# Performance work log

Measured on AMD Instinct MI355X. Metric: run time of the kernel, lower is better.

Reference implementation:

```python
import jax, jax.numpy as jnp
import numpy as np

N_NODES = 100000
N_EDGES = 1600000
UNITS = 256
N_LAYERS = 4          # model_layers
NUM_GRAPHS = 512
IN_FEAT = 9


def _glorot(key, shape):
    lim = float(np.sqrt(6.0 / (shape[0] + shape[1])))
    return jax.random.uniform(key, shape, jnp.float32, -lim, lim)


def setup_inputs() -> dict:
    key = jax.random.key(0)
    ks = jax.random.split(key, 16)
    x = jax.random.normal(ks[0], (N_NODES, IN_FEAT), jnp.float32)
    edge_index = jax.random.randint(ks[1], (2, N_EDGES), 0, N_NODES, jnp.int64)
    batch = jnp.sort(jax.random.randint(ks[2], (N_NODES,), 0, NUM_GRAPHS, jnp.int64))
    Win = _glorot(ks[3], (IN_FEAT, UNITS))
    bin_ = jnp.zeros((UNITS,), jnp.float32)
    Ws = jnp.stack([_glorot(ks[4 + i], (UNITS, UNITS)) for i in range(N_LAYERS - 1)])
    bs = jnp.zeros((N_LAYERS - 1, UNITS), jnp.float32)
    fc1_w = _glorot(ks[8], (UNITS, UNITS))
    fc1_b = jnp.zeros((UNITS,), jnp.float32)
    fc2_w = _glorot(ks[9], (UNITS, 32))
    fc2_b = jnp.zeros((32,), jnp.float32)
    fc3_w = _glorot(ks[10], (32, 1))
    fc3_b = jnp.zeros((1,), jnp.float32)
    return dict(x=x, edge_index=edge_index, batch=batch, Win=Win, bin_=bin_,
                Ws=Ws, bs=bs, fc1_w=fc1_w, fc1_b=fc1_b, fc2_w=fc2_w,
                fc2_b=fc2_b, fc3_w=fc3_w, fc3_b=fc3_b)


def _gcn_conv(x, W, b, src, dst, dinv):
    # PyG GCNConv: h = xW ; out = D^-1/2 (A+I) D^-1/2 h + b  (self-loops added)
    h = x @ W                                     # [N, d]
    norm = dinv[src] * dinv[dst]                  # [E]
    agg = jnp.zeros_like(h).at[dst].add(h[src] * norm[:, None])
    agg = agg + h * (dinv * dinv)[:, None]        # self-loop term
    return agg + b


def reference(x, edge_index, batch, Win, bin_, Ws, bs,
              fc1_w, fc1_b, fc2_w, fc2_b, fc3_w, fc3_b):
    src, dst = edge_index[0], edge_index[1]
    # degree with self-loops
    deg = jnp.zeros((N_NODES,), jnp.float32).at[dst].add(1.0) + 1.0
    dinv = jax.lax.rsqrt(deg)

    h = jnp.tanh(_gcn_conv(x, Win, bin_, src, dst, dinv))
    for i in range(N_LAYERS - 1):
        h = jnp.tanh(_gcn_conv(h, Ws[i], bs[i], src, dst, dinv))
        # dropout: identity at inference
    h = jnp.tanh(h @ fc1_w + fc1_b)
    h = jnp.tanh(h @ fc2_w + fc2_b)
    h = h @ fc3_w + fc3_b                          # [N, 1]
    # global mean pool over graphs
    sums = jax.ops.segment_sum(h, batch, num_segments=NUM_GRAPHS)      # [G, 1]
    cnts = jax.ops.segment_sum(jnp.ones((N_NODES,), jnp.float32), batch,
                               num_segments=NUM_GRAPHS)
    pooled = sums / jnp.maximum(cnts, 1.0)[:, None]
    return jax.nn.sigmoid(pooled)
```

## Files before the change

### kernel.cpp

```cpp
#include <hip/hip_runtime.h>
#include <math.h>

#define N_NODES 100000
#define N_EDGES 1600000
#define UNITS   256
#define NGRAPH  512
#define IN_FEAT 9
#define NB_SCAN ((N_NODES + 255) / 256)
#define NBUK    ((N_NODES + 255) / 256)
#define BCAP    8192
#define EPB     4096
#define NPB     ((N_EDGES + EPB - 1) / EPB)

typedef short bf16x8 __attribute__((ext_vector_type(8)));
typedef float f32x4  __attribute__((ext_vector_type(4)));
typedef float f32x2  __attribute__((ext_vector_type(2)));

__device__ __forceinline__ float bflo(unsigned int u) {
  return __builtin_bit_cast(float, u << 16);
}
__device__ __forceinline__ float bfhi(unsigned int u) {
  return __builtin_bit_cast(float, u & 0xffff0000u);
}
__device__ __forceinline__ unsigned short f2bf(float f) {
  unsigned int u = __builtin_bit_cast(unsigned int, f);
  u += 0x7fffu + ((u >> 16) & 1u);
  return (unsigned short)(u >> 16);
}

__device__ __forceinline__ bf16x8 f8tobf(uint2 q) {
  f32x2 v0 = __builtin_amdgcn_cvt_pk_f32_fp8(q.x, false);
  f32x2 v1 = __builtin_amdgcn_cvt_pk_f32_fp8(q.x, true);
  f32x2 v2 = __builtin_amdgcn_cvt_pk_f32_fp8(q.y, false);
  f32x2 v3 = __builtin_amdgcn_cvt_pk_f32_fp8(q.y, true);
  bf16x8 a;
  a[0] = (short)f2bf(v0[0]); a[1] = (short)f2bf(v0[1]);
  a[2] = (short)f2bf(v1[0]); a[3] = (short)f2bf(v1[1]);
  a[4] = (short)f2bf(v2[0]); a[5] = (short)f2bf(v2[1]);
  a[6] = (short)f2bf(v3[0]); a[7] = (short)f2bf(v3[1]);
  return a;
}

__device__ __forceinline__ int swz(int row, int byteInRow) {
  return row * 128 + (byteInRow ^ ((row & 7) << 4));
}
__device__ __forceinline__ int swzA(int row, int byteInRow) {
  return row * 512 + (byteInRow ^ ((row & 7) << 4));
}


__global__ __launch_bounds__(256) void k_part(const int* __restrict__ ei,
                                              int* __restrict__ bcnt,
                                              uint2* __restrict__ bstore) {
  __shared__ int hist[NBUK];
  __shared__ int base[NBUK];
  int tid = threadIdx.x;
  int e0 = blockIdx.x * EPB;
  for (int i = tid; i < NBUK; i += 256) hist[i] = 0;
  __syncthreads();
  #pragma unroll 4
  for (int j = 0; j < EPB / 256; ++j) {
    int e = e0 + j * 256 + tid;
    if (e < N_EDGES) atomicAdd(&hist[ei[N_EDGES + e] >> 8], 1);
  }
  __syncthreads();
  for (int i = tid; i < NBUK; i += 256) {
    int h = hist[i];
    base[i] = h ? atomicAdd(&bcnt[i], h) : 0;
    hist[i] = 0;
  }
  __syncthreads();
  #pragma unroll 4
  for (int j = 0; j < EPB / 256; ++j) {
    int e = e0 + j * 256 + tid;
    if (e < N_EDGES) {
      int s = ei[e];
      int d = ei[N_EDGES + e];
      int b = d >> 8;
      int pos = base[b] + atomicAdd(&hist[b], 1);
      bstore[(size_t)b * BCAP + pos] = make_uint2((unsigned)s, (unsigned)d);
    }
  }
}

__global__ __launch_bounds__(256) void k_cnt(const int* __restrict__ bcnt,
                                             const uint2* __restrict__ bstore,
                                             int* __restrict__ cnt) {
  __shared__ int h[256];
  int b = blockIdx.x, tid = threadIdx.x;
  h[tid] = 0;
  __syncthreads();
  int nE = bcnt[b];
  for (int i = tid; i < nE; i += 256)
    atomicAdd(&h[bstore[(size_t)b * BCAP + i].y & 255], 1);
  __syncthreads();
  int node = b * 256 + tid;
  if (node < N_NODES) cnt[node] = h[tid];
}

__global__ __launch_bounds__(256) void k_colfill(const int* __restrict__ bcnt,
                                                 const uint2* __restrict__ bstore,
                                                 const int* __restrict__ row_ptr,
                                                 int* __restrict__ col) {
  __shared__ int cur[256];
  int b = blockIdx.x, tid = threadIdx.x;
  int node = b * 256 + tid;
  cur[tid] = (node < N_NODES) ? row_ptr[node] : 0;
  __syncthreads();
  int nE = bcnt[b];
  for (int i = tid; i < nE; i += 256) {
    uint2 sd = bstore[(size_t)b * BCAP + i];
    int pos = atomicAdd(&cur[sd.y & 255], 1);
    col[pos] = (int)sd.x;
  }
}

__global__ __launch_bounds__(256) void k_bsum(const int* __restrict__ cnt,
                                              int* __restrict__ bsum) {
  __shared__ int wsS[4];
  int b = blockIdx.x, tid = threadIdx.x, lane = tid & 63, w = tid >> 6;
  int idx = b * 256 + tid;
  int s = (idx < N_NODES) ? cnt[idx] : 0;
  #pragma unroll
  for (int m = 32; m >= 1; m >>= 1) s += __shfl_xor(s, m);
  if (lane == 0) wsS[w] = s;
  __syncthreads();
  if (tid == 0) bsum[b] = wsS[0] + wsS[1] + wsS[2] + wsS[3];
}

__global__ __launch_bounds__(512) void k_bscan(int* __restrict__ bsum) {
  __shared__ int wsS[8];
  int tid = threadIdx.x, lane = tid & 63, w = tid >> 6;
  int v = (tid < NB_SCAN) ? bsum[tid] : 0;
  int s = v;
  #pragma unroll
  for (int off = 1; off < 64; off <<= 1) {
    int t = __shfl_up(s, off);
    if (lane >= off) s += t;
  }
  if (lane == 63) wsS[w] = s;
  __syncthreads();
  int woff = 0;
  #pragma unroll
  for (int i = 0; i < 8; ++i) woff += (i < w) ? wsS[i] : 0;
  if (tid < NB_SCAN) bsum[tid] = woff + s - v;
}

__global__ __launch_bounds__(256) void k_scan3(const int* __restrict__ cnt,
                                               const int* __restrict__ bsum,
                                               int* __restrict__ row_ptr,
                                               float* __restrict__ dinv) {
  __shared__ int wsS[4];
  int b = blockIdx.x, tid = threadIdx.x, lane = tid & 63, w = tid >> 6;
  int idx = b * 256 + tid;
  int v = (idx < N_NODES) ? cnt[idx] : 0;
  int s = v;
  #pragma unroll
  for (int off = 1; off < 64; off <<= 1) {
    int t = __shfl_up(s, off);
    if (lane >= off) s += t;
  }
  if (lane == 63) wsS[w] = s;
  __syncthreads();
  int woff = 0;
  #pragma unroll
  for (int i = 0; i < 4; ++i) woff += (i < w) ? wsS[i] : 0;
  if (idx < N_NODES) {
    row_ptr[idx] = bsum[b] + woff + s - v;
    dinv[idx] = rsqrtf((float)v + 1.0f);
  }
  if (idx == 0) row_ptr[N_NODES] = N_EDGES;
}

__global__ void k_bounds(const int* __restrict__ batch, int* __restrict__ starts) {
  int g = blockIdx.x * blockDim.x + threadIdx.x;
  if (g > NGRAPH) return;
  if (g == NGRAPH) { starts[g] = N_NODES; return; }
  int lo = 0, hi = N_NODES;
  while (lo < hi) { int m = (lo + hi) >> 1; if (batch[m] < g) lo = m + 1; else hi = m; }
  starts[g] = lo;
}


__global__ void k_cvtW(const float* __restrict__ Ws, const float* __restrict__ fc1_w,
                       unsigned short* __restrict__ Wt) {
  int idx = blockIdx.x * 256 + threadIdx.x;
  int m = idx >> 16;
  int r = idx & 65535;
  int n = r >> 8;
  int k = r & 255;
  const float* src = (m < 3) ? (Ws + (size_t)m * 65536) : fc1_w;
  Wt[idx] = f2bf(src[k * 256 + n]);
}

__global__ void k_cvtW2(const float* __restrict__ fc2_w, unsigned short* __restrict__ Wt2) {
  int idx = blockIdx.x * 256 + threadIdx.x;
  int n = idx >> 8;
  int k = idx & 255;
  Wt2[idx] = f2bf(fc2_w[k * 32 + n]);
}

__global__ void k_scalex(const float* __restrict__ x, const float* __restrict__ dinv,
                         float* __restrict__ xs) {
  int idx = blockIdx.x * blockDim.x + threadIdx.x;
  if (idx < N_NODES * IN_FEAT) xs[idx] = x[idx] * dinv[idx / IN_FEAT];
}


__global__ void k_agg9(const float* __restrict__ xs, const int* __restrict__ row_ptr,
                       const int* __restrict__ col, const float* __restrict__ dinv,
                       float* __restrict__ p0) {
  int n = blockIdx.x * blockDim.x + threadIdx.x;
  if (n >= N_NODES) return;
  float acc[IN_FEAT];
  #pragma unroll
  for (int j = 0; j < IN_FEAT; ++j) acc[j] = xs[n * IN_FEAT + j];
  int beg = row_ptr[n], end = row_ptr[n + 1];
  for (int e = beg; e < end; ++e) {
    int s = col[e];
    #pragma unroll
    for (int j = 0; j < IN_FEAT; ++j) acc[j] += xs[s * IN_FEAT + j];
  }
  float dn = dinv[n];
  #pragma unroll
  for (int j = 0; j < IN_FEAT; ++j) p0[n * IN_FEAT + j] = dn * acc[j];
}

__global__ __launch_bounds__(256) void k_gemm9(const float* __restrict__ p0,
                                               const float* __restrict__ Win,
                                               const float* __restrict__ bin,
                                               const float* __restrict__ scale,
                                               unsigned char* __restrict__ h8) {
  __shared__ float pS[32][IN_FEAT];
  int tid = threadIdx.x;
  int row0 = blockIdx.x * 32;
  for (int i = tid; i < 32 * IN_FEAT; i += 256) {
    int r = i / IN_FEAT;
    pS[r][i % IN_FEAT] = (row0 + r < N_NODES) ? p0[(size_t)row0 * IN_FEAT + i] : 0.0f;
  }
  float wcol[IN_FEAT];
  #pragma unroll
  for (int k = 0; k < IN_FEAT; ++k) wcol[k] = Win[k * UNITS + tid];
  float b = bin[tid];
  __syncthreads();
  for (int r = 0; r < 32; ++r) {
    int gr = row0 + r;
    if (gr >= N_NODES) break;
    float a = b;
    #pragma unroll
    for (int k = 0; k < IN_FEAT; ++k) a += pS[r][k] * wcol[k];
    float v = scale[gr] * tanhf(a);
    float vn = __shfl_xor(v, 1);
    if ((tid & 1) == 0) {
      unsigned int pk = __builtin_amdgcn_cvt_pk_fp8_f32(v, vn, 0, false);
      *(unsigned short*)(h8 + (size_t)gr * UNITS + tid) = (unsigned short)pk;
    }
  }
}


__global__ __launch_bounds__(256) void k_agg256(
    const unsigned int* __restrict__ hs8,
    const int* __restrict__ row_ptr, const int* __restrict__ col,
    const float* __restrict__ dinv, unsigned int* __restrict__ p8) {
  int wid = threadIdx.x >> 6;
  int lane = threadIdx.x & 63;
  int n = blockIdx.x * 4 + wid;
  if (n >= N_NODES) return;
  unsigned int q = hs8[(size_t)n * 64 + lane];
  f32x2 lo = __builtin_amdgcn_cvt_pk_f32_fp8(q, false);
  f32x2 hi = __builtin_amdgcn_cvt_pk_f32_fp8(q, true);
  float a0 = lo[0], a1 = lo[1], a2 = hi[0], a3 = hi[1];
  int e = row_ptr[n], end = row_ptr[n + 1];
  for (; e + 8 <= end; e += 8) {
    int s[8];
    unsigned int qq[8];
    #pragma unroll
    for (int j = 0; j < 8; ++j) s[j] = col[e + j];
    #pragma unroll
    for (int j = 0; j < 8; ++j) qq[j] = hs8[(size_t)s[j] * 64 + lane];
    #pragma unroll
    for (int j = 0; j < 8; ++j) {
      f32x2 l2 = __builtin_amdgcn_cvt_pk_f32_fp8(qq[j], false);
      f32x2 h2 = __builtin_amdgcn_cvt_pk_f32_fp8(qq[j], true);
      a0 += l2[0]; a1 += l2[1]; a2 += h2[0]; a3 += h2[1];
    }
  }
  if (e + 4 <= end) {
    int s[4];
    unsigned int qq[4];
    #pragma unroll
    for (int j = 0; j < 4; ++j) s[j] = col[e + j];
    #pragma unroll
    for (int j = 0; j < 4; ++j) qq[j] = hs8[(size_t)s[j] * 64 + lane];
    #pragma unroll
    for (int j = 0; j < 4; ++j) {
      f32x2 l2 = __builtin_amdgcn_cvt_pk_f32_fp8(qq[j], false);
      f32x2 h2 = __builtin_amdgcn_cvt_pk_f32_fp8(qq[j], true);
      a0 += l2[0]; a1 += l2[1]; a2 += h2[0]; a3 += h2[1];
    }
    e += 4;
  }
  for (; e < end; ++e) {
    unsigned int q0 = hs8[(size_t)col[e] * 64 + lane];
    f32x2 l2 = __builtin_amdgcn_cvt_pk_f32_fp8(q0, false);
    f32x2 h2 = __builtin_amdgcn_cvt_pk_f32_fp8(q0, true);
    a0 += l2[0]; a1 += l2[1]; a2 += h2[0]; a3 += h2[1];
  }
  float dn = dinv[n];
  unsigned int u = __builtin_amdgcn_cvt_pk_fp8_f32(dn * a0, dn * a1, 0, false);
  u = __builtin_amdgcn_cvt_pk_fp8_f32(dn * a2, dn * a3, u, true);
  p8[(size_t)n * 64 + lane] = u;
}


__global__ __launch_bounds__(256, 4) void k_gemm_f8(
    const unsigned char* __restrict__ A8,
    const unsigned short* __restrict__ Wt,
    const float* __restrict__ bias,
    const float* __restrict__ scale,
    unsigned char* __restrict__ C8,
    int M) {
  __shared__ __align__(16) char lds[33792];
  char* Bs = lds;
  unsigned short (*Cs)[264] = (unsigned short(*)[264])lds;

  const int tid = threadIdx.x;
  const int w = tid >> 6;
  const int l = tid & 63;
  const int l15 = l & 15;
  const int blk = l >> 4;
  const int wr = w >> 1, wc = w & 1;
  const int row0 = blockIdx.x * 64;

  const int sr = tid >> 3;
  const int sc = (tid & 7) * 16;

  const unsigned char* aRow[2];
  #pragma unroll
  for (int rf = 0; rf < 2; ++rf) {
    int gr = row0 + 32 * wr + rf * 16 + l15;
    if (gr >= M) gr = M - 1;
    aRow[rf] = A8 + (size_t)gr * UNITS + 8 * blk;
  }

  f32x4 acc[2][8];
  #pragma unroll
  for (int rf = 0; rf < 2; ++rf)
    #pragma unroll
    for (int cf = 0; cf < 8; ++cf) acc[rf][cf] = (f32x4){0.f, 0.f, 0.f, 0.f};

  for (int ks = 0; ks < 4; ++ks) {
    const int k0 = ks * 64;
    if (ks) __syncthreads();
    #pragma unroll
    for (int i = 0; i < 8; ++i) {
      int n = sr + i * 32;
      uint4 v = *(const uint4*)(Wt + (size_t)n * UNITS + k0 + (sc >> 1));
      *(uint4*)(Bs + swz(n, sc)) = v;
    }
    __syncthreads();
    #pragma unroll
    for (int kc = 0; kc < 2; ++kc) {
      bf16x8 a[2];
      #pragma unroll
      for (int rf = 0; rf < 2; ++rf) {
        uint2 q = *(const uint2*)(aRow[rf] + k0 + kc * 32);
        a[rf] = f8tobf(q);
      }
      #pragma unroll
      for (int cf = 0; cf < 8; ++cf) {
        bf16x8 b = *(const bf16x8*)(Bs + swz(128 * wc + cf * 16 + l15, kc * 64 + blk * 16));
        acc[0][cf] = __builtin_amdgcn_mfma_f32_16x16x32_bf16(a[0], b, acc[0][cf], 0, 0, 0);
        acc[1][cf] = __builtin_amdgcn_mfma_f32_16x16x32_bf16(a[1], b, acc[1][cf], 0, 0, 0);
      }
    }
  }

  __syncthreads();
  float dvv[2][4];
  #pragma unroll
  for (int rf = 0; rf < 2; ++rf)
    #pragma unroll
    for (int reg = 0; reg < 4; ++reg) {
      int gr = row0 + 32 * wr + rf * 16 + 4 * blk + reg;
      dvv[rf][reg] = scale[gr < M ? gr : M - 1];
    }
  #pragma unroll
  for (int cf = 0; cf < 8; ++cf) {
    float bcol = bias[128 * wc + cf * 16 + l15];
    #pragma unroll
    for (int rf = 0; rf < 2; ++rf) {
      #pragma unroll
      for (int reg = 0; reg < 4; ++reg) {
        float v = dvv[rf][reg] * tanhf(acc[rf][cf][reg] + bcol);
        Cs[32 * wr + rf * 16 + 4 * blk + reg][128 * wc + cf * 16 + l15] = f2bf(v);
      }
    }
  }
  __syncthreads();
  #pragma unroll
  for (int j = 0; j < 8; ++j) {
    int flat = tid + j * 256;
    int r = flat >> 5;
    int c = flat & 31;
    int gr = row0 + r;
    if (gr < M) {
      uint4 v = *(const uint4*)&Cs[r][c * 8];
      uint2 u;
      u.x = __builtin_amdgcn_cvt_pk_fp8_f32(bflo(v.x), bfhi(v.x), 0, false);
      u.x = __builtin_amdgcn_cvt_pk_fp8_f32(bflo(v.y), bfhi(v.y), u.x, true);
      u.y = __builtin_amdgcn_cvt_pk_fp8_f32(bflo(v.z), bfhi(v.z), 0, false);
      u.y = __builtin_amdgcn_cvt_pk_fp8_f32(bflo(v.w), bfhi(v.w), u.y, true);
      *(uint2*)(C8 + (size_t)gr * UNITS + c * 8) = u;
    }
  }
}


__global__ __launch_bounds__(256, 2) void k_mlp(
    const unsigned char* __restrict__ A8,
    const unsigned short* __restrict__ WtL2, const float* __restrict__ bL2,
    const unsigned short* __restrict__ Wtfc1, const float* __restrict__ bfc1,
    const unsigned short* __restrict__ Wt2, const float* __restrict__ b2,
    const float* __restrict__ w3, const float* __restrict__ b3,
    float* __restrict__ ns, int M) {
  __shared__ __align__(16) char lds[65536];
  char* T  = lds;
  char* Bs = lds + 32768;

  const int tid = threadIdx.x;
  const int w = tid >> 6;
  const int l = tid & 63;
  const int l15 = l & 15;
  const int blk = l >> 4;
  const int wr = w >> 1, wc = w & 1;
  const int row0 = blockIdx.x * 64;

  const int sr = tid >> 3;
  const int sc = (tid & 7) * 16;

  const unsigned char* aRow[2];
  #pragma unroll
  for (int rf = 0; rf < 2; ++rf) {
    int gr = row0 + 32 * wr + rf * 16 + l15;
    if (gr >= M) gr = M - 1;
    aRow[rf] = A8 + (size_t)gr * UNITS + 8 * blk;
  }
  f32x4 acc[2][8];
  #pragma unroll
  for (int rf = 0; rf < 2; ++rf)
    #pragma unroll
    for (int cf = 0; cf < 8; ++cf) acc[rf][cf] = (f32x4){0.f, 0.f, 0.f, 0.f};

  for (int ks = 0; ks < 4; ++ks) {
    const int k0 = ks * 64;
    if (ks) __syncthreads();
    #pragma unroll
    for (int i = 0; i < 8; ++i) {
      int n = sr + i * 32;
      uint4 v = *(const uint4*)(WtL2 + (size_t)n * UNITS + k0 + (sc >> 1));
      *(uint4*)(Bs + swz(n, sc)) = v;
    }
    __syncthreads();
    #pragma unroll
    for (int kc = 0; kc < 2; ++kc) {
      bf16x8 a[2];
      #pragma unroll
      for (int rf = 0; rf < 2; ++rf)
        a[rf] = f8tobf(*(const uint2*)(aRow[rf] + k0 + kc * 32));
      #pragma unroll
      for (int cf = 0; cf < 8; ++cf) {
        bf16x8 b = *(const bf16x8*)(Bs + swz(128 * wc + cf * 16 + l15, kc * 64 + blk * 16));
        acc[0][cf] = __builtin_amdgcn_mfma_f32_16x16x32_bf16(a[0], b, acc[0][cf], 0, 0, 0);
        acc[1][cf] = __builtin_amdgcn_mfma_f32_16x16x32_bf16(a[1], b, acc[1][cf], 0, 0, 0);
      }
    }
  }
  #pragma unroll
  for (int cf = 0; cf < 8; ++cf) {
    float bcol = bL2[128 * wc + cf * 16 + l15];
    #pragma unroll
    for (int rf = 0; rf < 2; ++rf) {
      #pragma unroll
      for (int reg = 0; reg < 4; ++reg) {
        int row = 32 * wr + rf * 16 + 4 * blk + reg;
        int colb = (128 * wc + cf * 16 + l15) * 2;
        *(unsigned short*)(T + swzA(row, colb)) = f2bf(tanhf(acc[rf][cf][reg] + bcol));
      }
    }
  }

  #pragma unroll
  for (int rf = 0; rf < 2; ++rf)
    #pragma unroll
    for (int cf = 0; cf < 8; ++cf) acc[rf][cf] = (f32x4){0.f, 0.f, 0.f, 0.f};
  for (int ks = 0; ks < 4; ++ks) {
    const int k0 = ks * 64;
    __syncthreads();
    #pragma unroll
    for (int i = 0; i < 8; ++i) {
      int n = sr + i * 32;
      uint4 v = *(const uint4*)(Wtfc1 + (size_t)n * UNITS + k0 + (sc >> 1));
      *(uint4*)(Bs + swz(n, sc)) = v;
    }
    __syncthreads();
    #pragma unroll
    for (int kc = 0; kc < 2; ++kc) {
      bf16x8 a[2];
      #pragma unroll
      for (int rf = 0; rf < 2; ++rf) {
        int ar = 32 * wr + rf * 16 + l15;
        a[rf] = *(const bf16x8*)(T + swzA(ar, blk * 16 + ks * 128 + kc * 64));
      }
      #pragma unroll
      for (int cf = 0; cf < 8; ++cf) {
        bf16x8 b = *(const bf16x8*)(Bs + swz(128 * wc + cf * 16 + l15, kc * 64 + blk * 16));
        acc[0][cf] = __builtin_amdgcn_mfma_f32_16x16x32_bf16(a[0], b, acc[0][cf], 0, 0, 0);
        acc[1][cf] = __builtin_amdgcn_mfma_f32_16x16x32_bf16(a[1], b, acc[1][cf], 0, 0, 0);
      }
    }
  }

  __syncthreads();
  #pragma unroll
  for (int cf = 0; cf < 8; ++cf) {
    float bcol = bfc1[128 * wc + cf * 16 + l15];
    #pragma unroll
    for (int rf = 0; rf < 2; ++rf) {
      #pragma unroll
      for (int reg = 0; reg < 4; ++reg) {
        int row = 32 * wr + rf * 16 + 4 * blk + reg;
        int colb = (128 * wc + cf * 16 + l15) * 2;
        *(unsigned short*)(T + swzA(row, colb)) = f2bf(tanhf(acc[rf][cf][reg] + bcol));
      }
    }
  }
  #pragma unroll
  for (int i = 0; i < 4; ++i) {
    int idx = tid + i * 256;
    int row = idx >> 5;
    int c = idx & 31;
    uint4 v = *(const uint4*)(Wt2 + (size_t)row * UNITS + c * 8);
    *(uint4*)(Bs + row * 512 + ((c * 16) ^ ((row & 7) << 4))) = v;
  }
  __syncthreads();

  f32x4 acc0 = (f32x4){0.f, 0.f, 0.f, 0.f};
  f32x4 acc1 = (f32x4){0.f, 0.f, 0.f, 0.f};
  #pragma unroll
  for (int k0 = 0; k0 < UNITS; k0 += 32) {
    int byte = k0 * 2 + blk * 16;
    bf16x8 a  = *(const bf16x8*)(T + swzA(16 * w + l15, byte));
    bf16x8 b0 = *(const bf16x8*)(Bs + l15 * 512 + (byte ^ ((l15 & 7) << 4)));
    bf16x8 b1 = *(const bf16x8*)(Bs + (16 + l15) * 512 + (byte ^ ((l15 & 7) << 4)));
    acc0 = __builtin_amdgcn_mfma_f32_16x16x32_bf16(a, b0, acc0, 0, 0, 0);
    acc1 = __builtin_amdgcn_mfma_f32_16x16x32_bf16(a, b1, acc1, 0, 0, 0);
  }
  float c0 = b2[l15], c1 = b2[16 + l15];
  float w30 = w3[l15], w31 = w3[16 + l15];
  float b3v = b3[0];
  #pragma unroll
  for (int reg = 0; reg < 4; ++reg) {
    float part = tanhf(acc0[reg] + c0) * w30 + tanhf(acc1[reg] + c1) * w31;
    #pragma unroll
    for (int m = 8; m >= 1; m >>= 1) part += __shfl_xor(part, m);
    int gr = row0 + 16 * w + 4 * blk + reg;
    if (l15 == 0 && gr < M) ns[gr] = part + b3v;
  }
}

__global__ __launch_bounds__(64) void k_pool(const float* __restrict__ ns,
                                             const int* __restrict__ starts,
                                             float* __restrict__ out) {
  int g = blockIdx.x;
  int lane = threadIdx.x;
  int s = starts[g], e = starts[g + 1];
  float acc = 0.0f;
  for (int i = s + lane; i < e; i += 64) acc += ns[i];
  #pragma unroll
  for (int m = 32; m >= 1; m >>= 1) acc += __shfl_xor(acc, m);
  if (lane == 0) {
    float mean = acc / fmaxf((float)(e - s), 1.0f);
    out[g] = 1.0f / (1.0f + expf(-mean));
  }
}


extern "C" void kernel_launch(void* const* d_in, const int* in_sizes, int n_in,
                              void* d_out, int out_size, void* d_ws, size_t ws_size,
                              hipStream_t stream) {
  const float* x     = (const float*)d_in[0];
  const int*   ei    = (const int*)d_in[1];
  const int*   batch = (const int*)d_in[2];
  const float* Win   = (const float*)d_in[3];
  const float* bin_  = (const float*)d_in[4];
  const float* Ws    = (const float*)d_in[5];
  const float* bs    = (const float*)d_in[6];
  const float* fc1_w = (const float*)d_in[7];
  const float* fc1_b = (const float*)d_in[8];
  const float* fc2_w = (const float*)d_in[9];
  const float* fc2_b = (const float*)d_in[10];
  const float* fc3_w = (const float*)d_in[11];
  const float* fc3_b = (const float*)d_in[12];
  float* out = (float*)d_out;

  char* ws = (char*)d_ws;
  size_t off = 0;
  auto alloc = [&](size_t bytes) {
    size_t o = off;
    off = (off + bytes + 255) & ~(size_t)255;
    return o;
  };
  int*   cnt     = (int*)(ws + alloc(N_NODES * 4));
  int*   row_ptr = (int*)(ws + alloc((N_NODES + 1) * 4));
  float* dinv    = (float*)(ws + alloc(N_NODES * 4));
  int*   col     = (int*)(ws + alloc((size_t)N_EDGES * 4));
  int*   bsum    = (int*)(ws + alloc(NB_SCAN * 4));
  int*   bcnt    = (int*)(ws + alloc(NBUK * 4));
  uint2* bstore  = (uint2*)(ws + alloc((size_t)NBUK * BCAP * 8));
  int*   starts  = (int*)(ws + alloc((NGRAPH + 1) * 4));
  float* ns      = (float*)(ws + alloc(N_NODES * 4));
  float* xs      = (float*)(ws + alloc((size_t)N_NODES * IN_FEAT * 4));
  float* p0      = (float*)(ws + alloc((size_t)N_NODES * IN_FEAT * 4));
  unsigned short* Wt   = (unsigned short*)(ws + alloc((size_t)4 * UNITS * UNITS * 2));
  unsigned short* Wt2  = (unsigned short*)(ws + alloc((size_t)32 * UNITS * 2));
  unsigned char*  h8a  = (unsigned char*)(ws + alloc((size_t)N_NODES * UNITS));
  unsigned char*  h8b  = (unsigned char*)(ws + alloc((size_t)N_NODES * UNITS));
  unsigned char*  p8   = (unsigned char*)(ws + alloc((size_t)N_NODES * UNITS));

  hipMemsetAsync(bcnt, 0, NBUK * 4, stream);

  k_cvtW<<<(4 * UNITS * UNITS) / 256, 256, 0, stream>>>(Ws, fc1_w, Wt);
  k_cvtW2<<<32, 256, 0, stream>>>(fc2_w, Wt2);

  k_part<<<NPB, 256, 0, stream>>>(ei, bcnt, bstore);
  k_cnt<<<NBUK, 256, 0, stream>>>(bcnt, bstore, cnt);
  k_bsum<<<NB_SCAN, 256, 0, stream>>>(cnt, bsum);
  k_bscan<<<1, 512, 0, stream>>>(bsum);
  k_scan3<<<NB_SCAN, 256, 0, stream>>>(cnt, bsum, row_ptr, dinv);
  k_colfill<<<NBUK, 256, 0, stream>>>(bcnt, bstore, row_ptr, col);
  k_bounds<<<3, 256, 0, stream>>>(batch, starts);

  k_scalex<<<(N_NODES * IN_FEAT + 255) / 256, 256, 0, stream>>>(x, dinv, xs);
  k_agg9<<<(N_NODES + 255) / 256, 256, 0, stream>>>(xs, row_ptr, col, dinv, p0);
  k_gemm9<<<(N_NODES + 31) / 32, 256, 0, stream>>>(p0, Win, bin_, dinv, h8a);

  int ggrid = (N_NODES + 63) / 64;
  k_agg256<<<(N_NODES + 3) / 4, 256, 0, stream>>>((const unsigned int*)h8a, row_ptr, col, dinv, (unsigned int*)p8);
  k_gemm_f8<<<ggrid, 256, 0, stream>>>(p8, Wt + (size_t)0 * UNITS * UNITS,
                                       bs + (size_t)0 * UNITS, dinv, h8b, N_NODES);
  k_agg256<<<(N_NODES + 3) / 4, 256, 0, stream>>>((const unsigned int*)h8b, row_ptr, col, dinv, (unsigned int*)p8);
  k_gemm_f8<<<ggrid, 256, 0, stream>>>(p8, Wt + (size_t)1 * UNITS * UNITS,
                                       bs + (size_t)1 * UNITS, dinv, h8a, N_NODES);
  k_agg256<<<(N_NODES + 3) / 4, 256, 0, stream>>>((const unsigned int*)h8a, row_ptr, col, dinv, (unsigned int*)p8);
  k_mlp<<<ggrid, 256, 0, stream>>>(p8, Wt + (size_t)2 * UNITS * UNITS,
                                   bs + (size_t)2 * UNITS,
                                   Wt + (size_t)3 * UNITS * UNITS, fc1_b,
                                   Wt2, fc2_b, fc3_w, fc3_b, ns, N_NODES);

  k_pool<<<NGRAPH, 64, 0, stream>>>(ns, starts, out);
}
```

Baseline: 497.7 us.

## Use fast tanh and store MLP intermediates as fp8 in LDS for higher occupancy

```diff
diff --git a/kernel.cpp b/kernel.cpp
--- a/kernel.cpp
+++ b/kernel.cpp
@@ -26,6 +26,11 @@
   unsigned int u = __builtin_bit_cast(unsigned int, f);
   u += 0x7fffu + ((u >> 16) & 1u);
   return (unsigned short)(u >> 16);
+}
+
+__device__ __forceinline__ float tanhfast(float x) {
+  float e = __expf(2.0f * x);
+  return 1.0f - 2.0f * __builtin_amdgcn_rcpf(e + 1.0f);
 }
 
 __device__ __forceinline__ bf16x8 f8tobf(uint2 q) {
@@ -40,12 +45,12 @@
   a[6] = (short)f2bf(v3[0]); a[7] = (short)f2bf(v3[1]);
   return a;
 }
+__device__ __forceinline__ unsigned char f2fp8(float v) {
+  return (unsigned char)(__builtin_amdgcn_cvt_pk_fp8_f32(v, v, 0, false) & 0xff);
+}
 
 __device__ __forceinline__ int swz(int row, int byteInRow) {
   return row * 128 + (byteInRow ^ ((row & 7) << 4));
-}
-__device__ __forceinline__ int swzA(int row, int byteInRow) {
-  return row * 512 + (byteInRow ^ ((row & 7) << 4));
 }
 
 
@@ -249,7 +254,7 @@
     float a = b;
     #pragma unroll
     for (int k = 0; k < IN_FEAT; ++k) a += pS[r][k] * wcol[k];
-    float v = scale[gr] * tanhf(a);
+    float v = scale[gr] * tanhfast(a);
     float vn = __shfl_xor(v, 1);
     if ((tid & 1) == 0) {
       unsigned int pk = __builtin_amdgcn_cvt_pk_fp8_f32(v, vn, 0, false);
@@ -393,7 +398,7 @@
     for (int rf = 0; rf < 2; ++rf) {
       #pragma unroll
       for (int reg = 0; reg < 4; ++reg) {
-        float v = dvv[rf][reg] * tanhf(acc[rf][cf][reg] + bcol);
+        float v = dvv[rf][reg] * tanhfast(acc[rf][cf][reg] + bcol);
         Cs[32 * wr + rf * 16 + 4 * blk + reg][128 * wc + cf * 16 + l15] = f2bf(v);
       }
     }
@@ -418,16 +423,16 @@
 }
 
 
-__global__ __launch_bounds__(256, 2) void k_mlp(
+__global__ __launch_bounds__(256, 3) void k_mlp(
     const unsigned char* __restrict__ A8,
     const unsigned short* __restrict__ WtL2, const float* __restrict__ bL2,
     const unsigned short* __restrict__ Wtfc1, const float* __restrict__ bfc1,
     const unsigned short* __restrict__ Wt2, const float* __restrict__ b2,
     const float* __restrict__ w3, const float* __restrict__ b3,
     float* __restrict__ ns, int M) {
-  __shared__ __align__(16) char lds[65536];
-  char* T  = lds;
-  char* Bs = lds + 32768;
+  __shared__ __align__(16) char lds[49152];
+  char* T8 = lds;
+  char* Bs = lds + 16384;
 
   const int tid = threadIdx.x;
   const int w = tid >> 6;
@@ -485,8 +490,8 @@
       #pragma unroll
       for (int reg = 0; reg < 4; ++reg) {
         int row = 32 * wr + rf * 16 + 4 * blk + reg;
-        int colb = (128 * wc + cf * 16 + l15) * 2;
-        *(unsigned short*)(T + swzA(row, colb)) = f2bf(tanhf(acc[rf][cf][reg] + bcol));
+        int colb = 128 * wc + cf * 16 + l15;
+        T8[row * 256 + (colb ^ ((row & 7) << 4))] = f2fp8(tanhfast(acc[rf][cf][reg] + bcol));
       }
     }
   }
@@ -511,7 +516,8 @@
       #pragma unroll
       for (int rf = 0; rf < 2; ++rf) {
         int ar = 32 * wr + rf * 16 + l15;
-        a[rf] = *(const bf16x8*)(T + swzA(ar, blk * 16 + ks * 128 + kc * 64));
+        int kb = k0 + kc * 32 + blk * 8;
+        a[rf] = f8tobf(*(const uint2*)(T8 + ar * 256 + (kb ^ ((ar & 7) << 4))));
       }
       #pragma unroll
       for (int cf = 0; cf < 8; ++cf) {
@@ -531,8 +537,8 @@
       #pragma unroll
       for (int reg = 0; reg < 4; ++reg) {
         int row = 32 * wr + rf * 16 + 4 * blk + reg;
-        int colb = (128 * wc + cf * 16 + l15) * 2;
-        *(unsigned short*)(T + swzA(row, colb)) = f2bf(tanhf(acc[rf][cf][reg] + bcol));
+        int colb = 128 * wc + cf * 16 + l15;
+        T8[row * 256 + (colb ^ ((row & 7) << 4))] = f2fp8(tanhfast(acc[rf][cf][reg] + bcol));
       }
     }
   }
@@ -550,8 +556,10 @@
   f32x4 acc1 = (f32x4){0.f, 0.f, 0.f, 0.f};
   #pragma unroll
   for (int k0 = 0; k0 < UNITS; k0 += 32) {
+    int ar = 16 * w + l15;
+    int kb = k0 + blk * 8;
+    bf16x8 a  = f8tobf(*(const uint2*)(T8 + ar * 256 + (kb ^ ((ar & 7) << 4))));
     int byte = k0 * 2 + blk * 16;
-    bf16x8 a  = *(const bf16x8*)(T + swzA(16 * w + l15, byte));
     bf16x8 b0 = *(const bf16x8*)(Bs + l15 * 512 + (byte ^ ((l15 & 7) << 4)));
     bf16x8 b1 = *(const bf16x8*)(Bs + (16 + l15) * 512 + (byte ^ ((l15 & 7) << 4)));
     acc0 = __builtin_amdgcn_mfma_f32_16x16x32_bf16(a, b0, acc0, 0, 0, 0);
@@ -562,7 +570,7 @@
   float b3v = b3[0];
   #pragma unroll
   for (int reg = 0; reg < 4; ++reg) {
-    float part = tanhf(acc0[reg] + c0) * w30 + tanhf(acc1[reg] + c1) * w31;
+    float part = tanhfast(acc0[reg] + c0) * w30 + tanhfast(acc1[reg] + c1) * w31;
     #pragma unroll
     for (int m = 8; m >= 1; m >>= 1) part += __shfl_xor(part, m);
     int gr = row0 + 16 * w + 4 * blk + reg;
```

Result: faster. 482.5 us, median of 2 (-3.0%).
